# Kernel tuning notes

Hardware: AMD Instinct MI355X
Metric: run time of the kernel (lower is better)

The kernel has to match this reference:

```python
import jax, jax.numpy as jnp
import numpy as np

B, S, D, H = 2, 2048, 768, 12
DK = D // H

def setup_inputs() -> dict:
    key = jax.random.key(0)
    ks = jax.random.split(key, 11)
    sc = 0.02
    inp = {
        'Q': jax.random.normal(ks[0], (B, S, D), jnp.float32),
        'K': jax.random.normal(ks[1], (B, S, D), jnp.float32),
        'V': jax.random.normal(ks[2], (B, S, D), jnp.float32),
        # causal mask, broadcastable over batch and heads (1 = keep, 0 = mask)
        'mask': jnp.tril(jnp.ones((S, S), jnp.int32))[None, None, :, :],
        'Wq': jax.random.normal(ks[3], (D, D), jnp.float32) * sc,
        'bq': jax.random.normal(ks[4], (D,), jnp.float32) * sc,
        'Wk': jax.random.normal(ks[5], (D, D), jnp.float32) * sc,
        'bk': jax.random.normal(ks[6], (D,), jnp.float32) * sc,
        'Wv': jax.random.normal(ks[7], (D, D), jnp.float32) * sc,
        'bv': jax.random.normal(ks[8], (D,), jnp.float32) * sc,
        'Wo': jax.random.normal(ks[9], (D, D), jnp.float32) * sc,
        'bo': jax.random.normal(ks[10], (D,), jnp.float32) * sc,
    }
    return inp

def _split_heads(x):
    # [B,S,D] -> [B,H,S,DK]
    return x.reshape(B, S, H, DK).transpose(0, 2, 1, 3)

def reference(Q, K, V, mask, Wq, bq, Wk, bk, Wv, bv, Wo, bo):
    # torch Linear: y = x @ W.T + b
    q = _split_heads(Q @ Wq.T + bq)
    k = _split_heads(K @ Wk.T + bk)
    v = _split_heads(V @ Wv.T + bv)
    scores = jnp.einsum('bhqd,bhkd->bhqk', q, k) / jnp.sqrt(jnp.float32(DK))
    scores = jnp.where(mask == 0, jnp.float32(-1e9), scores)
    attn = jax.nn.softmax(scores, axis=-1)
    out = jnp.einsum('bhqk,bhkd->bhqd', attn, v)  # [B,H,S,DK]
    out = out.transpose(0, 2, 1, 3).reshape(B, S, D)
    return out @ Wo.T + bo
```

## Files before the change

kernel.cpp:

```cpp
#include <hip/hip_runtime.h>
#include <hip/hip_bf16.h>

#define H_  12
#define S_  2048
#define D_  768
#define DK_ 64

typedef __bf16 bf16x8 __attribute__((ext_vector_type(8)));
typedef __bf16 bf16x4 __attribute__((ext_vector_type(4)));
typedef short  short4v __attribute__((ext_vector_type(4)));
typedef float  f32x4  __attribute__((ext_vector_type(4)));

#define QSCALE 0.1803368801111137f

__device__ inline float exp2_fast(float x) {
  return __builtin_amdgcn_exp2f(x);
}

__device__ inline f32x4 mfma_bf16(bf16x8 a, bf16x8 b, f32x4 c) {
  return __builtin_amdgcn_mfma_f32_16x16x32_bf16(a, b, c, 0, 0, 0);
}

__device__ inline f32x4 mfma16(bf16x4 a, bf16x4 b, f32x4 c) {
#if __has_builtin(__builtin_amdgcn_mfma_f32_16x16x16bf16_1k)
  short4v as = __builtin_bit_cast(short4v, a);
  short4v bs = __builtin_bit_cast(short4v, b);
  return __builtin_amdgcn_mfma_f32_16x16x16bf16_1k(as, bs, c, 0, 0, 0);
#else
  asm("s_nop 1\n\tv_mfma_f32_16x16x16_bf16 %0, %1, %2, %0"
      : "+v"(c) : "v"(a), "v"(b));
  return c;
#endif
}

__device__ inline void gload16(const void* g, void* l) {
  __builtin_amdgcn_global_load_lds(
      (const __attribute__((address_space(1))) void*)g,
      (__attribute__((address_space(3))) void*)l, 16, 0, 0);
}

__device__ inline bf16x8 cvt2bf16(f32x4 a, f32x4 b) {
  bf16x8 r;
  r[0] = (__bf16)a[0]; r[1] = (__bf16)a[1];
  r[2] = (__bf16)a[2]; r[3] = (__bf16)a[3];
  r[4] = (__bf16)b[0]; r[5] = (__bf16)b[1];
  r[6] = (__bf16)b[2]; r[7] = (__bf16)b[3];
  return r;
}

__global__ __launch_bounds__(256)
void conv_w(const float* __restrict__ Wq, const float* __restrict__ Wk,
            const float* __restrict__ Wv, const float* __restrict__ Wo,
            __hip_bfloat16* __restrict__ out)
{
  const int i8 = blockIdx.x * 256 + threadIdx.x;
  const int mat = i8 / 73728;
  const int off = (i8 - mat * 73728) * 8;
  const float* src = (mat == 0) ? Wq : (mat == 1) ? Wk : (mat == 2) ? Wv : Wo;
  f32x4 a = *(const f32x4*)(src + off);
  f32x4 b = *(const f32x4*)(src + off + 4);
  *(bf16x8*)(out + (size_t)mat * 589824 + off) = cvt2bf16(a, b);
}

__global__ __launch_bounds__(256, 3)
void qkv_proj(const float* __restrict__ Q, const float* __restrict__ K,
              const float* __restrict__ V,
              const __hip_bfloat16* __restrict__ Wb,
              const float* __restrict__ bq, const float* __restrict__ bk,
              const float* __restrict__ bv,
              __hip_bfloat16* __restrict__ q_ws,
              __hip_bfloat16* __restrict__ k_ws,
              __hip_bfloat16* __restrict__ vT_ws)
{
  __shared__ alignas(16) __hip_bfloat16 Ald[128 * 32];
  __shared__ alignas(16) __hip_bfloat16 Bld[128 * 32];

  const int z = blockIdx.z;
  const float* X    = (z == 0) ? Q  : (z == 1) ? K  : V;
  const float* bias = (z == 0) ? bq : (z == 1) ? bk : bv;
  const __hip_bfloat16* Wz = Wb + (size_t)z * 589824;
  __hip_bfloat16* out = (z == 0) ? q_ws : (z == 1) ? k_ws : vT_ws;
  const bool vmode = (z == 2);
  const float osc = (z == 0) ? QSCALE : 1.0f;

  const int t    = threadIdx.x;
  const int w    = t >> 6;
  const int lane = t & 63;
  const int l15  = lane & 15;
  const int quad = lane >> 4;
  const int m0 = blockIdx.x * 128;
  const int n0 = blockIdx.y * 128;
  const int wm = (w >> 1) * 64;
  const int wn = (w & 1) * 64;

  __hip_bfloat16* Xbuf = vmode ? Bld : Ald;
  __hip_bfloat16* Wbuf = vmode ? Ald : Bld;

  const f32x4 fzero = {0.f, 0.f, 0.f, 0.f};
  f32x4 acc[4][4];
#pragma unroll
  for (int i = 0; i < 4; ++i)
#pragma unroll
    for (int j = 0; j < 4; ++j) acc[i][j] = fzero;

  const int ar = t >> 2, ac = t & 3;
  const int sw = ac ^ ((ar >> 1) & 3);
  const float* As0 = X + (size_t)(m0 + ar) * D_ + ac * 8;
  const float* As1 = X + (size_t)(m0 + ar + 64) * D_ + ac * 8;
  __hip_bfloat16* Xw0 = &Xbuf[((ar)      * 4 + sw) * 8];
  __hip_bfloat16* Xw1 = &Xbuf[((ar + 64) * 4 + sw) * 8];

  const int bp = (t & 3) ^ (((t >> 2) >> 1) & 3);
  const __hip_bfloat16* Bs0 = Wz + (size_t)(n0 + (t >> 2)) * D_ + bp * 8;
  const __hip_bfloat16* Bs1 = Wz + (size_t)(n0 + (t >> 2) + 64) * D_ + bp * 8;
  __hip_bfloat16* Wd0 = &Wbuf[t * 8];
  __hip_bfloat16* Wd1 = &Wbuf[(t + 256) * 8];

  int agrn[4], bgrn[4];
#pragma unroll
  for (int i = 0; i < 4; ++i) {
    int row = wm + 16 * i + l15;
    agrn[i] = (row * 4 + (quad ^ ((row >> 1) & 3))) * 8;
    row = wn + 16 * i + l15;
    bgrn[i] = (row * 4 + (quad ^ ((row >> 1) & 3))) * 8;
  }

  f32x4 a00 = *(const f32x4*)As0, a01 = *(const f32x4*)(As0 + 4);
  f32x4 a10 = *(const f32x4*)As1, a11 = *(const f32x4*)(As1 + 4);

  for (int k0 = 0; k0 < D_; k0 += 32) {
    *(bf16x8*)Xw0 = cvt2bf16(a00, a01);
    *(bf16x8*)Xw1 = cvt2bf16(a10, a11);
    gload16(Bs0 + k0, Wd0);
    gload16(Bs1 + k0, Wd1);
    __syncthreads();

    const int kn = k0 + 32;
    if (kn < D_) {
      a00 = *(const f32x4*)(As0 + kn); a01 = *(const f32x4*)(As0 + kn + 4);
      a10 = *(const f32x4*)(As1 + kn); a11 = *(const f32x4*)(As1 + kn + 4);
    }

    bf16x8 af[4], bfr[4];
#pragma unroll
    for (int i = 0; i < 4; ++i) af[i]  = *(const bf16x8*)&Ald[agrn[i]];
#pragma unroll
    for (int j = 0; j < 4; ++j) bfr[j] = *(const bf16x8*)&Bld[bgrn[j]];
#pragma unroll
    for (int i = 0; i < 4; ++i)
#pragma unroll
      for (int j = 0; j < 4; ++j)
        acc[i][j] = mfma_bf16(af[i], bfr[j], acc[i][j]);
    __syncthreads();
  }

  if (!vmode) {
#pragma unroll
    for (int j = 0; j < 4; ++j) {
      const int n_g = n0 + wn + 16 * j + l15;
      const float bv = bias[n_g];
      const int hh = n_g >> 6, dk = n_g & (DK_ - 1);
#pragma unroll
      for (int i = 0; i < 4; ++i) {
        const int mbase = m0 + wm + 16 * i + quad * 4;
#pragma unroll
        for (int r = 0; r < 4; ++r) {
          const int m_g = mbase + r;
          const int bb = m_g >> 11, ss = m_g & (S_ - 1);
          const float vout = (acc[i][j][r] + bv) * osc;
          out[(((size_t)(bb * H_ + hh)) * S_ + ss) * DK_ + dk] =
              __float2bfloat16(vout);
        }
      }
    }
  } else {
#pragma unroll
    for (int i = 0; i < 4; ++i) {
      const int nbase = n0 + wm + 16 * i + quad * 4;
#pragma unroll
      for (int r = 0; r < 4; ++r) {
        const int n_g = nbase + r;
        const float bv = bias[n_g];
        const int hh = n_g >> 6, dk = n_g & (DK_ - 1);
#pragma unroll
        for (int j = 0; j < 4; ++j) {
          const int m_g = m0 + wn + 16 * j + l15;
          const int bb = m_g >> 11, ss = m_g & (S_ - 1);
          out[(((size_t)(bb * H_ + hh)) * DK_ + dk) * S_ + ss] =
              __float2bfloat16(acc[i][j][r] + bv);
        }
      }
    }
  }
}

__global__ __launch_bounds__(256, 4)
void o_proj(const __hip_bfloat16* __restrict__ Xb,
            const __hip_bfloat16* __restrict__ Wob,
            const float* __restrict__ bias,
            float* __restrict__ outf)
{
  __shared__ alignas(16) __hip_bfloat16 Ald[64 * 32];
  __shared__ alignas(16) __hip_bfloat16 Bld[128 * 32];

  const int t    = threadIdx.x;
  const int w    = t >> 6;
  const int lane = t & 63;
  const int l15  = lane & 15;
  const int quad = lane >> 4;
  const int m0 = blockIdx.x * 64;
  const int n0 = blockIdx.y * 128;
  const int wm = (w >> 1) * 32;
  const int wn = (w & 1) * 64;

  const f32x4 fzero = {0.f, 0.f, 0.f, 0.f};
  f32x4 acc[2][4];
#pragma unroll
  for (int i = 0; i < 2; ++i)
#pragma unroll
    for (int j = 0; j < 4; ++j) acc[i][j] = fzero;

  const int ap = (t & 3) ^ (((t >> 2) >> 1) & 3);
  const __hip_bfloat16* As  = Xb  + (size_t)(m0 + (t >> 2)) * D_ + ap * 8;
  const __hip_bfloat16* Bs0 = Wob + (size_t)(n0 + (t >> 2)) * D_ + ap * 8;
  const __hip_bfloat16* Bs1 = Wob + (size_t)(n0 + (t >> 2) + 64) * D_ + ap * 8;
  __hip_bfloat16* Ad  = &Ald[t * 8];
  __hip_bfloat16* Bd0 = &Bld[t * 8];
  __hip_bfloat16* Bd1 = &Bld[(t + 256) * 8];

  int agrn[2], bgrn[4];
#pragma unroll
  for (int i = 0; i < 2; ++i) {
    const int row = wm + 16 * i + l15;
    agrn[i] = (row * 4 + (quad ^ ((row >> 1) & 3))) * 8;
  }
#pragma unroll
  for (int j = 0; j < 4; ++j) {
    const int row = wn + 16 * j + l15;
    bgrn[j] = (row * 4 + (quad ^ ((row >> 1) & 3))) * 8;
  }

  for (int k0 = 0; k0 < D_; k0 += 32) {
    gload16(As + k0, Ad);
    gload16(Bs0 + k0, Bd0);
    gload16(Bs1 + k0, Bd1);
    __syncthreads();

    bf16x8 af[2], bfr[4];
#pragma unroll
    for (int i = 0; i < 2; ++i) af[i]  = *(const bf16x8*)&Ald[agrn[i]];
#pragma unroll
    for (int j = 0; j < 4; ++j) bfr[j] = *(const bf16x8*)&Bld[bgrn[j]];
#pragma unroll
    for (int i = 0; i < 2; ++i)
#pragma unroll
      for (int j = 0; j < 4; ++j)
        acc[i][j] = mfma_bf16(af[i], bfr[j], acc[i][j]);
    __syncthreads();
  }

#pragma unroll
  for (int j = 0; j < 4; ++j) {
    const int n_g = n0 + wn + 16 * j + l15;
    const float bv = bias[n_g];
#pragma unroll
    for (int i = 0; i < 2; ++i) {
      const int mbase = m0 + wm + 16 * i + quad * 4;
#pragma unroll
      for (int r = 0; r < 4; ++r)
        outf[(size_t)(mbase + r) * D_ + n_g] = acc[i][j][r] + bv;
    }
  }
}

__global__ __launch_bounds__(256, 4)
void flash_attn(const __hip_bfloat16* __restrict__ q_ws,
                const __hip_bfloat16* __restrict__ k_ws,
                const __hip_bfloat16* __restrict__ vT_ws,
                __hip_bfloat16* __restrict__ o_ws)
{
  __shared__ alignas(16) __hip_bfloat16 Kld[128][72];
  __shared__ alignas(16) __hip_bfloat16 Vld[64][136];

  const int t = threadIdx.x, w = t >> 6, lane = t & 63;
  const int l15 = lane & 15, quad = lane >> 4;

  const int id   = blockIdx.x;
  const int slot = id & 7;
  const int jj   = id >> 3;
  const int grp  = jj >> 5;
  const int bh   = slot + 8 * grp;
  const int x    = ((jj & 31) + 13 * grp) & 31;

  const int b = bh / H_, h = bh % H_;
  const int tLo = x, tHi = 63 - x;
  const int myTile = (w < 2) ? tLo : tHi;
  const int qbase = myTile * 32 + 16 * (w & 1);
  const int qg = qbase + l15;
  const int myNkt = (myTile >> 2) + 1;
  const int nktT  = (tHi >> 2) + 1;
  const size_t hbase = (size_t)bh * S_ * DK_;
  const size_t vtb   = (size_t)bh * DK_ * S_;

  bf16x8 qf[2];
#pragma unroll
  for (int kk = 0; kk < 2; ++kk)
    qf[kk] = *(const bf16x8*)(q_ws + hbase + (size_t)qg * DK_ + kk * 32 + quad * 8);

  const f32x4 fzero = {0.f, 0.f, 0.f, 0.f};
  f32x4 accO[4];
#pragma unroll
  for (int jd = 0; jd < 4; ++jd) accO[jd] = fzero;
  float mI = -1.0e30f, lI = 0.f;

  const int tr = t >> 3, kg = t & 7;
  const int tv = t >> 4, vg = t & 15;
  const __hip_bfloat16* Kbase = k_ws + hbase + (size_t)tr * DK_ + kg * 8;
  const __hip_bfloat16* Vbase = vT_ws + vtb + (size_t)tv * S_ + vg * 8;

  bf16x8 rK[4], rV[4];
#pragma unroll
  for (int it = 0; it < 4; ++it) {
    rK[it] = *(const bf16x8*)(Kbase + (size_t)(32 * it) * DK_);
    rV[it] = *(const bf16x8*)(Vbase + (size_t)(16 * it) * S_);
  }

  for (int kt = 0; kt < nktT; ++kt) {
#pragma unroll
    for (int it = 0; it < 4; ++it) {
      *(bf16x8*)&Kld[32 * it + tr][kg * 8] = rK[it];
      *(bf16x8*)&Vld[16 * it + tv][vg * 8] = rV[it];
    }
    __syncthreads();

    if (kt + 1 < nktT) {
      const int k0n = (kt + 1) * 128;
#pragma unroll
      for (int it = 0; it < 4; ++it) {
        rK[it] = *(const bf16x8*)(Kbase + (size_t)(k0n + 32 * it) * DK_);
        rV[it] = *(const bf16x8*)(Vbase + (size_t)(16 * it) * S_ + k0n);
      }
    }

    if (kt < myNkt) {
      const int k0 = kt * 128;
      f32x4 st[8];
#pragma unroll
      for (int j = 0; j < 8; ++j) {
        bf16x8 kf0 = *(const bf16x8*)&Kld[16 * j + l15][quad * 8];
        bf16x8 kf1 = *(const bf16x8*)&Kld[16 * j + l15][32 + quad * 8];
        st[j] = mfma_bf16(kf0, qf[0], fzero);
        st[j] = mfma_bf16(kf1, qf[1], st[j]);
      }

      if (kt == myNkt - 1) {
#pragma unroll
        for (int j = 0; j < 8; ++j)
#pragma unroll
          for (int r = 0; r < 4; ++r) {
            const int kcg = k0 + 16 * j + quad * 4 + r;
            if (kcg > qg) st[j][r] = -1.0e9f;
          }
      }

      float tm = st[0][0];
#pragma unroll
      for (int j = 0; j < 8; ++j)
#pragma unroll
        for (int r = 0; r < 4; ++r) tm = fmaxf(tm, st[j][r]);
      tm = fmaxf(tm, __shfl_xor(tm, 16));
      tm = fmaxf(tm, __shfl_xor(tm, 32));

      const float mnew = fmaxf(mI, tm);
      const float al = exp2_fast(mI - mnew);
      mI = mnew;
      float rs = 0.f;
#pragma unroll
      for (int j = 0; j < 8; ++j)
#pragma unroll
        for (int r = 0; r < 4; ++r) {
          const float pv = exp2_fast(st[j][r] - mnew);
          st[j][r] = pv;
          rs += pv;
        }
      rs += __shfl_xor(rs, 16);
      rs += __shfl_xor(rs, 32);
      lI = lI * al + rs;
#pragma unroll
      for (int jd = 0; jd < 4; ++jd)
#pragma unroll
        for (int r = 0; r < 4; ++r) accO[jd][r] *= al;

      bf16x4 pb[8];
#pragma unroll
      for (int j = 0; j < 8; ++j) {
        pb[j][0] = (__bf16)st[j][0]; pb[j][1] = (__bf16)st[j][1];
        pb[j][2] = (__bf16)st[j][2]; pb[j][3] = (__bf16)st[j][3];
      }

#pragma unroll
      for (int jd = 0; jd < 4; ++jd)
#pragma unroll
        for (int j = 0; j < 8; ++j) {
          bf16x4 vf = *(const bf16x4*)&Vld[16 * jd + l15][16 * j + quad * 4];
          accO[jd] = mfma16(vf, pb[j], accO[jd]);
        }
    }
    __syncthreads();
  }

  const float inv = 1.f / lI;
#pragma unroll
  for (int jd = 0; jd < 4; ++jd) {
    bf16x4 ov;
#pragma unroll
    for (int r = 0; r < 4; ++r) ov[r] = (__bf16)(accO[jd][r] * inv);
    *(bf16x4*)(o_ws + ((size_t)b * S_ + qg) * D_ + h * DK_ + 16 * jd + quad * 4) = ov;
  }
}

extern "C" void kernel_launch(void* const* d_in, const int* in_sizes, int n_in,
                              void* d_out, int out_size, void* d_ws, size_t ws_size,
                              hipStream_t stream) {
  (void)in_sizes; (void)n_in; (void)out_size; (void)ws_size;
  const float* Q  = (const float*)d_in[0];
  const float* K  = (const float*)d_in[1];
  const float* V  = (const float*)d_in[2];
  const float* Wq = (const float*)d_in[4];
  const float* bq = (const float*)d_in[5];
  const float* Wk = (const float*)d_in[6];
  const float* bk = (const float*)d_in[7];
  const float* Wv = (const float*)d_in[8];
  const float* bv = (const float*)d_in[9];
  const float* Wo = (const float*)d_in[10];
  const float* bo = (const float*)d_in[11];
  float* out = (float*)d_out;

  const size_t WEL = (size_t)4 * 589824;
  const size_t NEL = (size_t)2 * S_ * D_;
  __hip_bfloat16* wb    = (__hip_bfloat16*)d_ws;
  __hip_bfloat16* q_ws  = wb + WEL;
  __hip_bfloat16* k_ws  = q_ws  + NEL;
  __hip_bfloat16* vT_ws = k_ws  + NEL;
  __hip_bfloat16* o_ws  = vT_ws + NEL;

  conv_w<<<1152, 256, 0, stream>>>(Wq, Wk, Wv, Wo, wb);
  qkv_proj<<<dim3(32, 6, 3), 256, 0, stream>>>(Q, K, V, wb, bq, bk, bv,
                                               q_ws, k_ws, vT_ws);
  flash_attn<<<768, 256, 0, stream>>>(q_ws, k_ws, vT_ws, o_ws);
  o_proj<<<dim3(64, 6), 256, 0, stream>>>(o_ws, wb + (size_t)3 * 589824, bo, out);
}
```

Measured before the change: 194.9 us.

## Use 16x16x32 MFMA for PV with permuted V^T layout and wave priorities

The V-projection kernel now writes V^T with a permuted sequence index inside each 32-column group. This lets the attention kernel load 8 contiguous bf16 values per lane and run the P·V product with the wider 16x16x32 bf16 MFMA instead of twice as many 16x16x16 MFMAs. MFMA sections are also bracketed with s_setprio, and the assignment of low/high query tiles to waves is flipped by tile parity to balance causal work across SIMDs. The permutation has to match exactly between the producer and the consumer, or the results will be wrong.

```diff
diff --git a/kernel.cpp b/kernel.cpp
--- a/kernel.cpp
+++ b/kernel.cpp
@@ -8,7 +8,6 @@
 
 typedef __bf16 bf16x8 __attribute__((ext_vector_type(8)));
 typedef __bf16 bf16x4 __attribute__((ext_vector_type(4)));
-typedef short  short4v __attribute__((ext_vector_type(4)));
 typedef float  f32x4  __attribute__((ext_vector_type(4)));
 
 #define QSCALE 0.1803368801111137f
@@ -19,18 +18,6 @@
 
 __device__ inline f32x4 mfma_bf16(bf16x8 a, bf16x8 b, f32x4 c) {
   return __builtin_amdgcn_mfma_f32_16x16x32_bf16(a, b, c, 0, 0, 0);
-}
-
-__device__ inline f32x4 mfma16(bf16x4 a, bf16x4 b, f32x4 c) {
-#if __has_builtin(__builtin_amdgcn_mfma_f32_16x16x16bf16_1k)
-  short4v as = __builtin_bit_cast(short4v, a);
-  short4v bs = __builtin_bit_cast(short4v, b);
-  return __builtin_amdgcn_mfma_f32_16x16x16bf16_1k(as, bs, c, 0, 0, 0);
-#else
-  asm("s_nop 1\n\tv_mfma_f32_16x16x16_bf16 %0, %1, %2, %0"
-      : "+v"(c) : "v"(a), "v"(b));
-  return c;
-#endif
 }
 
 __device__ inline void gload16(const void* g, void* l) {
@@ -186,7 +173,9 @@
         for (int j = 0; j < 4; ++j) {
           const int m_g = m0 + wn + 16 * j + l15;
           const int bb = m_g >> 11, ss = m_g & (S_ - 1);
-          out[(((size_t)(bb * H_ + hh)) * DK_ + dk) * S_ + ss] =
+          const int ssp = (ss & ~31) | (((ss >> 2) & 3) << 3) |
+                          (((ss >> 4) & 1) << 2) | (ss & 3);
+          out[(((size_t)(bb * H_ + hh)) * DK_ + dk) * S_ + ssp] =
               __float2bfloat16(acc[i][j][r] + bv);
         }
       }
@@ -294,7 +283,8 @@
 
   const int b = bh / H_, h = bh % H_;
   const int tLo = x, tHi = 63 - x;
-  const int myTile = (w < 2) ? tLo : tHi;
+  const int flip = x & 1;
+  const int myTile = ((w >> 1) ^ flip) ? tHi : tLo;
   const int qbase = myTile * 32 + 16 * (w & 1);
   const int qg = qbase + l15;
   const int myNkt = (myTile >> 2) + 1;
@@ -345,6 +335,7 @@
     if (kt < myNkt) {
       const int k0 = kt * 128;
       f32x4 st[8];
+      __builtin_amdgcn_s_setprio(1);
 #pragma unroll
       for (int j = 0; j < 8; ++j) {
         bf16x8 kf0 = *(const bf16x8*)&Kld[16 * j + l15][quad * 8];
@@ -352,6 +343,7 @@
         st[j] = mfma_bf16(kf0, qf[0], fzero);
         st[j] = mfma_bf16(kf1, qf[1], st[j]);
       }
+      __builtin_amdgcn_s_setprio(0);
 
       if (kt == myNkt - 1) {
 #pragma unroll
@@ -391,20 +383,24 @@
 #pragma unroll
         for (int r = 0; r < 4; ++r) accO[jd][r] *= al;
 
-      bf16x4 pb[8];
-#pragma unroll
-      for (int j = 0; j < 8; ++j) {
-        pb[j][0] = (__bf16)st[j][0]; pb[j][1] = (__bf16)st[j][1];
-        pb[j][2] = (__bf16)st[j][2]; pb[j][3] = (__bf16)st[j][3];
-      }
-
-#pragma unroll
-      for (int jd = 0; jd < 4; ++jd)
-#pragma unroll
-        for (int j = 0; j < 8; ++j) {
-          bf16x4 vf = *(const bf16x4*)&Vld[16 * jd + l15][16 * j + quad * 4];
-          accO[jd] = mfma16(vf, pb[j], accO[jd]);
+      bf16x8 pB[4];
+#pragma unroll
+      for (int s = 0; s < 4; ++s)
+#pragma unroll
+        for (int i = 0; i < 4; ++i) {
+          pB[s][i]     = (__bf16)st[2 * s][i];
+          pB[s][4 + i] = (__bf16)st[2 * s + 1][i];
         }
+
+      __builtin_amdgcn_s_setprio(1);
+#pragma unroll
+      for (int s = 0; s < 4; ++s)
+#pragma unroll
+        for (int jd = 0; jd < 4; ++jd) {
+          bf16x8 vf = *(const bf16x8*)&Vld[16 * jd + l15][32 * s + quad * 8];
+          accO[jd] = mfma_bf16(vf, pB[s], accO[jd]);
+        }
+      __builtin_amdgcn_s_setprio(0);
     }
     __syncthreads();
   }
```

Result: faster. 189.9 us (-2.6%).
